# Optimization experiments

Measured on AMD Instinct MI355X. Metric: run time of the kernel, lower is better.

The kernel has to match this reference:

```python
import jax, jax.numpy as jnp
import numpy as np

R = 64                      # grid resolution
SCALE = 1.05                # half-extent of the grid
C = 64                      # feature_dim
N = 500_000                 # number of query positions
GRID_SIZE = SCALE * 2.0 / R


def _build_grid():
    """Regular (R+1)^3 vertex grid spanning [-SCALE, SCALE]^3 plus per-cube
    8-corner vertex indices, with binary corner ordering c = 4*dx + 2*dy + dz
    so corner 7-c is the diagonally opposite corner (needed for flip(-2))."""
    R1 = R + 1
    lin = (np.arange(R1, dtype=np.float32) / R - 0.5) * (2.0 * SCALE)
    gx, gy, gz = np.meshgrid(lin, lin, lin, indexing='ij')
    vertices = np.stack([gx, gy, gz], axis=-1).reshape(-1, 3)  # [(R+1)^3, 3]
    i, j, k = np.meshgrid(np.arange(R), np.arange(R), np.arange(R), indexing='ij')
    corners = []
    for c in range(8):
        dx, dy, dz = (c >> 2) & 1, (c >> 1) & 1, c & 1
        corners.append((i + dx) * R1 * R1 + (j + dy) * R1 + (k + dz))
    grid_indices = np.stack(corners, axis=-1).astype(np.int32)  # [R, R, R, 8]
    return jnp.asarray(vertices), jnp.asarray(grid_indices)


def setup_inputs() -> dict:
    key = jax.random.key(0)
    k1, k2 = jax.random.split(key)
    vertices, grid_indices = _build_grid()
    # query positions uniform in [-SCALE, SCALE]^3
    positions = (jax.random.uniform(k1, (N, 3), dtype=jnp.float32) * 2.0 - 1.0) * SCALE
    # learned feature grid, init like torch.randn(...) * init_std
    feats = jax.random.normal(k2, ((R + 1) ** 3, C), dtype=jnp.float32) * 0.001
    return {"positions": positions, "feats": feats,
            "vertices": vertices, "grid_indices": grid_indices}


def reference(positions, feats, vertices, grid_indices):
    # NeuFAM.trilinear_query
    x = jnp.clip((positions / (2.0 * SCALE) + 0.5) * R, 0.0, float(R))
    nearest = jnp.clip(jnp.floor(x).astype(jnp.int32), 0, R - 1)          # [N, 3]
    idx = grid_indices[nearest[:, 0], nearest[:, 1], nearest[:, 2]]       # [N, 8]
    verts = vertices[idx]                                                 # [N, 8, 3]
    nf = feats[idx]                                                       # [N, 8, C]
    # trilinear weight = prod over xyz of |p - opposite corner| / grid_size
    w = jnp.prod(jnp.abs((positions[:, None, :] - verts[:, ::-1, :]) / GRID_SIZE), axis=-1)  # [N, 8]
    return jnp.einsum('nkc,nk->nc', nf, w)                                # [N, C]
```

## Files before the change

kernel.cpp:

```cpp
#include <hip/hip_runtime.h>
#include <hip/hip_fp16.h>


#define GRID_R     64
#define GRID_R1    65
#define NCHAN      64
#define NVERT      (GRID_R1 * GRID_R1 * GRID_R1)
#define FEAT_ELEMS ((size_t)NVERT * NCHAN)
#define NBINS      512
#define REPS       64

typedef float    f32x4 __attribute__((ext_vector_type(4)));
typedef _Float16 f16x8 __attribute__((ext_vector_type(8)));

__device__ __forceinline__ void cell_of(float px, float py, float pz,
                                        int& ci, int& cj, int& ck) {
    float x = (px / 2.1f + 0.5f) * 64.0f;
    float y = (py / 2.1f + 0.5f) * 64.0f;
    float z = (pz / 2.1f + 0.5f) * 64.0f;
    x = fminf(fmaxf(x, 0.0f), 64.0f);
    y = fminf(fmaxf(y, 0.0f), 64.0f);
    z = fminf(fmaxf(z, 0.0f), 64.0f);
    ci = min((int)x, GRID_R - 1);
    cj = min((int)y, GRID_R - 1);
    ck = min((int)z, GRID_R - 1);
}

__device__ __forceinline__ int sbin_of(int ci, int cj, int ck) {
    return ((ci >> 3) << 6) | ((cj >> 3) << 3) | (ck >> 3);
}

__global__ __launch_bounds__(256) void convert_hist_kernel(
    const f32x4* __restrict__ in,
    f16x8* __restrict__ outF,
    const float* __restrict__ pos,
    int* __restrict__ hist,
    int n8, int n)
{
    int i = blockIdx.x * 256 + threadIdx.x;
    if (i < n8) {
        f32x4 a = __builtin_nontemporal_load(&in[2 * i]);
        f32x4 b = __builtin_nontemporal_load(&in[2 * i + 1]);
        f16x8 h;
        h[0] = (_Float16)a.x; h[1] = (_Float16)a.y;
        h[2] = (_Float16)a.z; h[3] = (_Float16)a.w;
        h[4] = (_Float16)b.x; h[5] = (_Float16)b.y;
        h[6] = (_Float16)b.z; h[7] = (_Float16)b.w;
        __builtin_nontemporal_store(h, &outF[i]);
    }
    if (i < n) {
        int ci, cj, ck;
        cell_of(pos[i * 3], pos[i * 3 + 1], pos[i * 3 + 2], ci, cj, ck);
        const int rep = blockIdx.x & (REPS - 1);
        atomicAdd(&hist[rep * NBINS + sbin_of(ci, cj, ck)], 1);
    }
}

__global__ __launch_bounds__(NBINS) void scan_kernel(
    const int* __restrict__ hist,
    int* __restrict__ cursor)
{
    __shared__ int s[NBINS];
    const int t = threadIdx.x;
    int pre[REPS];
    int tot = 0;
#pragma unroll
    for (int r = 0; r < REPS; ++r) { pre[r] = tot; tot += hist[r * NBINS + t]; }
    s[t] = tot;
    __syncthreads();
    for (int off = 1; off < NBINS; off <<= 1) {
        int v = (t >= off) ? s[t - off] : 0;
        __syncthreads();
        s[t] += v;
        __syncthreads();
    }
    const int base = s[t] - tot;
#pragma unroll
    for (int r = 0; r < REPS; ++r) cursor[r * NBINS + t] = base + pre[r];
}

__global__ __launch_bounds__(256) void scatter_kernel(
    const float* __restrict__ pos,
    int* __restrict__ cursor,
    f32x4* __restrict__ records,
    int n)
{
    int i = blockIdx.x * 256 + threadIdx.x;
    if (i >= n) return;
    float px = pos[i * 3], py = pos[i * 3 + 1], pz = pos[i * 3 + 2];
    int ci, cj, ck;
    cell_of(px, py, pz, ci, cj, ck);
    const int rep = blockIdx.x & (REPS - 1);
    int slot = atomicAdd(&cursor[rep * NBINS + sbin_of(ci, cj, ck)], 1);
    f32x4 r = {px, py, pz, __int_as_float(i)};
    __builtin_nontemporal_store(r, &records[slot]);
}

__global__ __launch_bounds__(256) void trilerp_sorted_kernel(
    const f32x4* __restrict__ records,
    const f16x8* __restrict__ feats,
    f32x4* __restrict__ out4,
    int n, int nwg)
{
    const int o  = blockIdx.x;
    const int x  = o & 7, oo = o >> 3;
    const int q  = nwg >> 3, r = nwg & 7;
    const int vb = (x < r ? x * (q + 1) : r * (q + 1) + (x - r) * q) + oo;

    const int slot = vb * 32 + (threadIdx.x >> 3);
    if (slot >= n) return;
    const int sub = threadIdx.x & 7;

    const f32x4 rec = records[slot];
    const float px = rec.x, py = rec.y, pz = rec.z;
    const int orig = __float_as_int(rec.w);

    int ci, cj, ck;
    cell_of(px, py, pz, ci, cj, ck);

    const float INV_GS = 64.0f / 2.1f;
    float vx0 = ((float)ci       * 0.015625f - 0.5f) * 2.1f;
    float vx1 = ((float)(ci + 1) * 0.015625f - 0.5f) * 2.1f;
    float vy0 = ((float)cj       * 0.015625f - 0.5f) * 2.1f;
    float vy1 = ((float)(cj + 1) * 0.015625f - 0.5f) * 2.1f;
    float vz0 = ((float)ck       * 0.015625f - 0.5f) * 2.1f;
    float vz1 = ((float)(ck + 1) * 0.015625f - 0.5f) * 2.1f;

    float wx1 = fabsf(px - vx0) * INV_GS;
    float wx0 = fabsf(px - vx1) * INV_GS;
    float wy1 = fabsf(py - vy0) * INV_GS;
    float wy0 = fabsf(py - vy1) * INV_GS;
    float wz1 = fabsf(pz - vz0) * INV_GS;
    float wz0 = fabsf(pz - vz1) * INV_GS;

    const int RS = NCHAN / 8;
    const int SY = GRID_R1 * RS;
    const int SX = GRID_R1 * GRID_R1 * RS;
    int base = ((ci * GRID_R1 + cj) * GRID_R1 + ck) * RS + sub;

    f16x8 f000 = feats[base];
    f16x8 f001 = feats[base + RS];
    f16x8 f010 = feats[base + SY];
    f16x8 f011 = feats[base + SY + RS];
    f16x8 f100 = feats[base + SX];
    f16x8 f101 = feats[base + SX + RS];
    f16x8 f110 = feats[base + SX + SY];
    f16x8 f111 = feats[base + SX + SY + RS];

    float w000 = wx0 * wy0 * wz0, w001 = wx0 * wy0 * wz1;
    float w010 = wx0 * wy1 * wz0, w011 = wx0 * wy1 * wz1;
    float w100 = wx1 * wy0 * wz0, w101 = wx1 * wy0 * wz1;
    float w110 = wx1 * wy1 * wz0, w111 = wx1 * wy1 * wz1;

    f32x4 acc0 = {0.f, 0.f, 0.f, 0.f};
    f32x4 acc1 = {0.f, 0.f, 0.f, 0.f};
#define ACCUM(F, W)                                                  \
    { acc0.x += (float)F[0] * W; acc0.y += (float)F[1] * W;          \
      acc0.z += (float)F[2] * W; acc0.w += (float)F[3] * W;          \
      acc1.x += (float)F[4] * W; acc1.y += (float)F[5] * W;          \
      acc1.z += (float)F[6] * W; acc1.w += (float)F[7] * W; }
    ACCUM(f000, w000) ACCUM(f001, w001) ACCUM(f010, w010) ACCUM(f011, w011)
    ACCUM(f100, w100) ACCUM(f101, w101) ACCUM(f110, w110) ACCUM(f111, w111)
#undef ACCUM

    __builtin_nontemporal_store(acc0, &out4[orig * 16 + sub * 2]);
    __builtin_nontemporal_store(acc1, &out4[orig * 16 + sub * 2 + 1]);
}

__global__ __launch_bounds__(256) void trilerp_f16_kernel(
    const float* __restrict__ pos,
    const f16x8* __restrict__ feats,
    f32x4* __restrict__ out4,
    int n)
{
    const int tid = blockIdx.x * 256 + threadIdx.x;
    const int pt  = tid >> 3;
    if (pt >= n) return;
    const int sub = tid & 7;

    const float px = pos[pt * 3], py = pos[pt * 3 + 1], pz = pos[pt * 3 + 2];
    int ci, cj, ck;
    cell_of(px, py, pz, ci, cj, ck);

    const float INV_GS = 64.0f / 2.1f;
    float vx0 = ((float)ci       * 0.015625f - 0.5f) * 2.1f;
    float vx1 = ((float)(ci + 1) * 0.015625f - 0.5f) * 2.1f;
    float vy0 = ((float)cj       * 0.015625f - 0.5f) * 2.1f;
    float vy1 = ((float)(cj + 1) * 0.015625f - 0.5f) * 2.1f;
    float vz0 = ((float)ck       * 0.015625f - 0.5f) * 2.1f;
    float vz1 = ((float)(ck + 1) * 0.015625f - 0.5f) * 2.1f;

    float wx1 = fabsf(px - vx0) * INV_GS;
    float wx0 = fabsf(px - vx1) * INV_GS;
    float wy1 = fabsf(py - vy0) * INV_GS;
    float wy0 = fabsf(py - vy1) * INV_GS;
    float wz1 = fabsf(pz - vz0) * INV_GS;
    float wz0 = fabsf(pz - vz1) * INV_GS;

    const int RS = NCHAN / 8, SY = GRID_R1 * RS, SX = GRID_R1 * GRID_R1 * RS;
    int base = ((ci * GRID_R1 + cj) * GRID_R1 + ck) * RS + sub;

    f16x8 f000 = feats[base];
    f16x8 f001 = feats[base + RS];
    f16x8 f010 = feats[base + SY];
    f16x8 f011 = feats[base + SY + RS];
    f16x8 f100 = feats[base + SX];
    f16x8 f101 = feats[base + SX + RS];
    f16x8 f110 = feats[base + SX + SY];
    f16x8 f111 = feats[base + SX + SY + RS];

    float w000 = wx0 * wy0 * wz0, w001 = wx0 * wy0 * wz1;
    float w010 = wx0 * wy1 * wz0, w011 = wx0 * wy1 * wz1;
    float w100 = wx1 * wy0 * wz0, w101 = wx1 * wy0 * wz1;
    float w110 = wx1 * wy1 * wz0, w111 = wx1 * wy1 * wz1;

    f32x4 acc0 = {0.f, 0.f, 0.f, 0.f};
    f32x4 acc1 = {0.f, 0.f, 0.f, 0.f};
#define ACCUM(F, W)                                                  \
    { acc0.x += (float)F[0] * W; acc0.y += (float)F[1] * W;          \
      acc0.z += (float)F[2] * W; acc0.w += (float)F[3] * W;          \
      acc1.x += (float)F[4] * W; acc1.y += (float)F[5] * W;          \
      acc1.z += (float)F[6] * W; acc1.w += (float)F[7] * W; }
    ACCUM(f000, w000) ACCUM(f001, w001) ACCUM(f010, w010) ACCUM(f011, w011)
    ACCUM(f100, w100) ACCUM(f101, w101) ACCUM(f110, w110) ACCUM(f111, w111)
#undef ACCUM

    __builtin_nontemporal_store(acc0, &out4[pt * 16 + sub * 2]);
    __builtin_nontemporal_store(acc1, &out4[pt * 16 + sub * 2 + 1]);
}

__global__ __launch_bounds__(256) void trilerp_f32_kernel(
    const float* __restrict__ pos,
    const f32x4* __restrict__ feats4,
    f32x4* __restrict__ out4,
    int n)
{
    const int tid = blockIdx.x * 256 + threadIdx.x;
    const int pt  = tid >> 4;
    if (pt >= n) return;
    const int sub = tid & 15;

    const float px = pos[pt * 3], py = pos[pt * 3 + 1], pz = pos[pt * 3 + 2];
    int ci, cj, ck;
    cell_of(px, py, pz, ci, cj, ck);

    const float INV_GS = 64.0f / 2.1f;
    float vx0 = ((float)ci       * 0.015625f - 0.5f) * 2.1f;
    float vx1 = ((float)(ci + 1) * 0.015625f - 0.5f) * 2.1f;
    float vy0 = ((float)cj       * 0.015625f - 0.5f) * 2.1f;
    float vy1 = ((float)(cj + 1) * 0.015625f - 0.5f) * 2.1f;
    float vz0 = ((float)ck       * 0.015625f - 0.5f) * 2.1f;
    float vz1 = ((float)(ck + 1) * 0.015625f - 0.5f) * 2.1f;

    float wx1 = fabsf(px - vx0) * INV_GS;
    float wx0 = fabsf(px - vx1) * INV_GS;
    float wy1 = fabsf(py - vy0) * INV_GS;
    float wy0 = fabsf(py - vy1) * INV_GS;
    float wz1 = fabsf(pz - vz0) * INV_GS;
    float wz0 = fabsf(pz - vz1) * INV_GS;

    const int RS = 16, SY = GRID_R1 * RS, SX = GRID_R1 * GRID_R1 * RS;
    int base = ((ci * GRID_R1 + cj) * GRID_R1 + ck) * RS + sub;

    f32x4 f000 = feats4[base];
    f32x4 f001 = feats4[base + RS];
    f32x4 f010 = feats4[base + SY];
    f32x4 f011 = feats4[base + SY + RS];
    f32x4 f100 = feats4[base + SX];
    f32x4 f101 = feats4[base + SX + RS];
    f32x4 f110 = feats4[base + SX + SY];
    f32x4 f111 = feats4[base + SX + SY + RS];

    float w000 = wx0 * wy0 * wz0, w001 = wx0 * wy0 * wz1;
    float w010 = wx0 * wy1 * wz0, w011 = wx0 * wy1 * wz1;
    float w100 = wx1 * wy0 * wz0, w101 = wx1 * wy0 * wz1;
    float w110 = wx1 * wy1 * wz0, w111 = wx1 * wy1 * wz1;

    f32x4 acc = f000 * w000 + f001 * w001 + f010 * w010 + f011 * w011
              + f100 * w100 + f101 * w101 + f110 * w110 + f111 * w111;

    __builtin_nontemporal_store(acc, &out4[pt * 16 + sub]);
}

extern "C" void kernel_launch(void* const* d_in, const int* in_sizes, int n_in,
                              void* d_out, int out_size, void* d_ws, size_t ws_size,
                              hipStream_t stream) {
    const float* pos   = (const float*)d_in[0];
    const float* feats = (const float*)d_in[1];
    f32x4* out4 = (f32x4*)d_out;

    const int n  = in_sizes[0] / 3;
    const int n8 = (int)(FEAT_ELEMS / 8);

    const size_t featBytes = FEAT_ELEMS * sizeof(_Float16);
    const size_t offF = 0;
    const size_t offR = (featBytes + 127) & ~(size_t)127;
    const size_t offH = offR + (size_t)n * 16;
    const size_t offC = offH + (size_t)REPS * NBINS * sizeof(int);
    const size_t needSorted = offC + (size_t)REPS * NBINS * sizeof(int);

    if (ws_size >= needSorted) {
        char* ws = (char*)d_ws;
        f16x8* feats16 = (f16x8*)(ws + offF);
        f32x4* records = (f32x4*)(ws + offR);
        int*   hist    = (int*)(ws + offH);
        int*   cursor  = (int*)(ws + offC);

        hipMemsetAsync(hist, 0, (size_t)REPS * NBINS * sizeof(int), stream);

        const int k1_blocks = (n8 + 255) / 256;
        convert_hist_kernel<<<k1_blocks, 256, 0, stream>>>(
            (const f32x4*)feats, feats16, pos, hist, n8, n);

        scan_kernel<<<1, NBINS, 0, stream>>>(hist, cursor);

        scatter_kernel<<<(n + 255) / 256, 256, 0, stream>>>(
            pos, cursor, records, n);

        const int nwg = (n + 31) / 32;
        trilerp_sorted_kernel<<<nwg, 256, 0, stream>>>(
            records, feats16, out4, n, nwg);
    } else if (ws_size >= featBytes) {
        f16x8* feats16 = (f16x8*)d_ws;
        convert_hist_kernel<<<(n8 + 255) / 256, 256, 0, stream>>>(
            (const f32x4*)feats, feats16, nullptr, nullptr, n8, 0);
        const long long total = (long long)n * 8;
        trilerp_f16_kernel<<<(int)((total + 255) / 256), 256, 0, stream>>>(
            pos, feats16, out4, n);
    } else {
        const long long total = (long long)n * 16;
        trilerp_f32_kernel<<<(int)((total + 255) / 256), 256, 0, stream>>>(
            pos, (const f32x4*)feats, out4, n);
    }
}
```

Measured before the change: 127.4 us.

## Sort queries into fine 2x2x2-cell bins instead of replicated coarse super-bins

Replaces the 512 coarse 8^3-cell super-bins, each replicated 64 ways to spread atomic contention, with 32768 fine bins covering 2x2x2 cells each and no replication. The scan kernel now uses 1024 threads that each sum 32 consecutive bins. Sorting more finely should give the gather kernel tighter locality on feature vertices. The cost is more contention on the histogram and cursor atomics, since same-bin points now land on the same counter, plus less ordered scatter writes. The fallback f32 kernel is also rewritten as a loop over corners, which is only a cosmetic change.

```diff
diff --git a/kernel.cpp b/kernel.cpp
--- a/kernel.cpp
+++ b/kernel.cpp
@@ -7,8 +7,7 @@
 #define NCHAN      64
 #define NVERT      (GRID_R1 * GRID_R1 * GRID_R1)
 #define FEAT_ELEMS ((size_t)NVERT * NCHAN)
-#define NBINS      512
-#define REPS       64
+#define NBIN2      32768
 
 typedef float    f32x4 __attribute__((ext_vector_type(4)));
 typedef _Float16 f16x8 __attribute__((ext_vector_type(8)));
@@ -26,8 +25,8 @@
     ck = min((int)z, GRID_R - 1);
 }
 
-__device__ __forceinline__ int sbin_of(int ci, int cj, int ck) {
-    return ((ci >> 3) << 6) | ((cj >> 3) << 3) | (ck >> 3);
+__device__ __forceinline__ int bin_of(int ci, int cj, int ck) {
+    return ((ci >> 1) << 10) | ((cj >> 1) << 5) | (ck >> 1);
 }
 
 __global__ __launch_bounds__(256) void convert_hist_kernel(
@@ -51,24 +50,23 @@
     if (i < n) {
         int ci, cj, ck;
         cell_of(pos[i * 3], pos[i * 3 + 1], pos[i * 3 + 2], ci, cj, ck);
-        const int rep = blockIdx.x & (REPS - 1);
-        atomicAdd(&hist[rep * NBINS + sbin_of(ci, cj, ck)], 1);
+        atomicAdd(&hist[bin_of(ci, cj, ck)], 1);
     }
 }
 
-__global__ __launch_bounds__(NBINS) void scan_kernel(
+__global__ __launch_bounds__(1024) void scan_kernel(
     const int* __restrict__ hist,
     int* __restrict__ cursor)
 {
-    __shared__ int s[NBINS];
+    __shared__ int s[1024];
     const int t = threadIdx.x;
-    int pre[REPS];
+    int pre[32];
     int tot = 0;
 #pragma unroll
-    for (int r = 0; r < REPS; ++r) { pre[r] = tot; tot += hist[r * NBINS + t]; }
+    for (int i = 0; i < 32; ++i) { pre[i] = tot; tot += hist[t * 32 + i]; }
     s[t] = tot;
     __syncthreads();
-    for (int off = 1; off < NBINS; off <<= 1) {
+    for (int off = 1; off < 1024; off <<= 1) {
         int v = (t >= off) ? s[t - off] : 0;
         __syncthreads();
         s[t] += v;
@@ -76,7 +74,7 @@
     }
     const int base = s[t] - tot;
 #pragma unroll
-    for (int r = 0; r < REPS; ++r) cursor[r * NBINS + t] = base + pre[r];
+    for (int i = 0; i < 32; ++i) cursor[t * 32 + i] = base + pre[i];
 }
 
 __global__ __launch_bounds__(256) void scatter_kernel(
@@ -90,8 +88,7 @@
     float px = pos[i * 3], py = pos[i * 3 + 1], pz = pos[i * 3 + 2];
     int ci, cj, ck;
     cell_of(px, py, pz, ci, cj, ck);
-    const int rep = blockIdx.x & (REPS - 1);
-    int slot = atomicAdd(&cursor[rep * NBINS + sbin_of(ci, cj, ck)], 1);
+    int slot = atomicAdd(&cursor[bin_of(ci, cj, ck)], 1);
     f32x4 r = {px, py, pz, __int_as_float(i)};
     __builtin_nontemporal_store(r, &records[slot]);
 }
@@ -252,32 +249,19 @@
     float vz0 = ((float)ck       * 0.015625f - 0.5f) * 2.1f;
     float vz1 = ((float)(ck + 1) * 0.015625f - 0.5f) * 2.1f;
 
-    float wx1 = fabsf(px - vx0) * INV_GS;
-    float wx0 = fabsf(px - vx1) * INV_GS;
-    float wy1 = fabsf(py - vy0) * INV_GS;
-    float wy0 = fabsf(py - vy1) * INV_GS;
-    float wz1 = fabsf(pz - vz0) * INV_GS;
-    float wz0 = fabsf(pz - vz1) * INV_GS;
+    float wx1 = fabsf(px - vx0) * INV_GS, wx0 = fabsf(px - vx1) * INV_GS;
+    float wy1 = fabsf(py - vy0) * INV_GS, wy0 = fabsf(py - vy1) * INV_GS;
+    float wz1 = fabsf(pz - vz0) * INV_GS, wz0 = fabsf(pz - vz1) * INV_GS;
+    float w[8] = {wx0*wy0*wz0, wx0*wy0*wz1, wx0*wy1*wz0, wx0*wy1*wz1,
+                  wx1*wy0*wz0, wx1*wy0*wz1, wx1*wy1*wz0, wx1*wy1*wz1};
 
     const int RS = 16, SY = GRID_R1 * RS, SX = GRID_R1 * GRID_R1 * RS;
-    int base = ((ci * GRID_R1 + cj) * GRID_R1 + ck) * RS + sub;
-
-    f32x4 f000 = feats4[base];
-    f32x4 f001 = feats4[base + RS];
-    f32x4 f010 = feats4[base + SY];
-    f32x4 f011 = feats4[base + SY + RS];
-    f32x4 f100 = feats4[base + SX];
-    f32x4 f101 = feats4[base + SX + RS];
-    f32x4 f110 = feats4[base + SX + SY];
-    f32x4 f111 = feats4[base + SX + SY + RS];
-
-    float w000 = wx0 * wy0 * wz0, w001 = wx0 * wy0 * wz1;
-    float w010 = wx0 * wy1 * wz0, w011 = wx0 * wy1 * wz1;
-    float w100 = wx1 * wy0 * wz0, w101 = wx1 * wy0 * wz1;
-    float w110 = wx1 * wy1 * wz0, w111 = wx1 * wy1 * wz1;
-
-    f32x4 acc = f000 * w000 + f001 * w001 + f010 * w010 + f011 * w011
-              + f100 * w100 + f101 * w101 + f110 * w110 + f111 * w111;
+    const int off[8] = {0, RS, SY, SY + RS, SX, SX + RS, SX + SY, SX + SY + RS};
+    int b = ((ci * GRID_R1 + cj) * GRID_R1 + ck) * 16 + sub;
+
+    f32x4 acc = {0.f, 0.f, 0.f, 0.f};
+#pragma unroll
+    for (int c = 0; c < 8; ++c) acc += feats4[b + off[c]] * w[c];
 
     __builtin_nontemporal_store(acc, &out4[pt * 16 + sub]);
 }
@@ -296,8 +280,8 @@
     const size_t offF = 0;
     const size_t offR = (featBytes + 127) & ~(size_t)127;
     const size_t offH = offR + (size_t)n * 16;
-    const size_t offC = offH + (size_t)REPS * NBINS * sizeof(int);
-    const size_t needSorted = offC + (size_t)REPS * NBINS * sizeof(int);
+    const size_t offC = offH + (size_t)NBIN2 * sizeof(int);
+    const size_t needSorted = offC + (size_t)NBIN2 * sizeof(int);
 
     if (ws_size >= needSorted) {
         char* ws = (char*)d_ws;
@@ -306,13 +290,12 @@
         int*   hist    = (int*)(ws + offH);
         int*   cursor  = (int*)(ws + offC);
 
-        hipMemsetAsync(hist, 0, (size_t)REPS * NBINS * sizeof(int), stream);
-
-        const int k1_blocks = (n8 + 255) / 256;
-        convert_hist_kernel<<<k1_blocks, 256, 0, stream>>>(
+        hipMemsetAsync(hist, 0, (size_t)NBIN2 * sizeof(int), stream);
+
+        convert_hist_kernel<<<(n8 + 255) / 256, 256, 0, stream>>>(
             (const f32x4*)feats, feats16, pos, hist, n8, n);
 
-        scan_kernel<<<1, NBINS, 0, stream>>>(hist, cursor);
+        scan_kernel<<<1, 1024, 0, stream>>>(hist, cursor);
 
         scatter_kernel<<<(n + 255) / 256, 256, 0, stream>>>(
             pos, cursor, records, n);
```

Result: slower. 151.3 us (+18.7%).
